# Kernel tuning notes

Hardware: AMD Instinct MI355X
Metric: run time of the kernel (lower is better)

Reference implementation:

```python
import math
import jax, jax.numpy as jnp
import numpy as np

B, L, D = 8, 512, 512          # batch, seq, d_model
G, S = 8, 4                    # n_groups, expert_scale (clones per group)
FG, FE = 4, 64                 # features per group, d_feat_emb
E = G * S                      # n_experts = 32
DH, RH = 256, 256              # d_expert_hidden, d_router_hidden
TEMP, SHARP, BIAS = 1.0, 16.0, 1.0
GK, SK = 2, 2                  # group_top_k, expert_top_k


def setup_inputs() -> dict:
    key = jax.random.key(0)
    ks = jax.random.split(key, 12)
    def n(k, shape, fan_in):
        return (jax.random.normal(k, shape) * (fan_in ** -0.5)).astype(jnp.float32)
    return {
        "hidden": jax.random.normal(ks[0], (B, L, D), jnp.float32),
        "feat": jax.random.uniform(ks[1], (B, L, G * FG), dtype=jnp.float32),
        "valid_mask": jnp.ones((B, L), jnp.bool_),
        # outer (group) router: hidden -> RH -> G
        "Wr1": n(ks[2], (D, RH), D), "br1": jnp.zeros((RH,), jnp.float32),
        "Wr2": n(ks[3], (RH, G), RH), "br2": jnp.zeros((G,), jnp.float32),
        # per-group feature embedding: FG -> FE
        "Wfe": n(ks[4], (G, FG, FE), FG), "bfe": jnp.zeros((G, FE), jnp.float32),
        # per-group inner (clone) router on [hidden ; feat_emb] -> S
        "Win_h": n(ks[5], (G, D, S), D + FE),
        "Win_f": n(ks[6], (G, FE, S), D + FE),
        "bin_b": jnp.zeros((G, S), jnp.float32),
        # per-expert MLP: D -> DH -> D
        "We1": n(ks[7], (E, D, DH), D), "be1": jnp.zeros((E, DH), jnp.float32),
        "We2": n(ks[8], (E, DH, D), DH), "be2": jnp.zeros((E, D), jnp.float32),
    }


def _to_ratio(x):
    # faithful to _to_ratio: clamp if already in [0,1], else Gaussian CDF
    clamped = jnp.clip(x, 0.0, 1.0)
    cdf = jnp.clip(0.5 * (1.0 + jax.lax.erf(x / math.sqrt(2.0))), 0.0, 1.0)
    in01 = jnp.logical_and(x.min() >= -1e-6, x.max() <= 1.0 + 1e-6)
    return jnp.where(in01, clamped, cdf)


def _topk_softmax(logits, k):
    # softmax over top-k entries, zeros elsewhere (== scatter of softmax(top_vals))
    vals, _ = jax.lax.top_k(logits, k)
    thresh = vals[..., -1:]
    neg = jnp.finfo(logits.dtype).min
    return jax.nn.softmax(jnp.where(logits >= thresh, logits, neg), axis=-1)


def _forward(hidden, feat, Wr1, br1, Wr2, br2, Wfe, bfe, Win_h, Win_f, bin_b,
             We1, be1, We2, be2):
    gelu = lambda x: jax.nn.gelu(x, approximate=False)  # torch nn.GELU default
    # ---- outer (group) router: hidden-only, token mode ----
    gh = gelu(hidden @ Wr1 + br1)                       # [B,L,RH]
    glog = (gh @ Wr2 + br2) / TEMP                      # [B,L,G]
    gw = _topk_softmax(glog, GK)                        # [B,L,G]
    # ---- inner rule teacher: bins over normalized group feature ratios ----
    feat_g = feat.reshape(B, L, G, FG)
    score = _to_ratio(feat_g).mean(-1, keepdims=True)   # [B,L,G,1]
    centers = jnp.linspace(0.0, 1.0, S, dtype=jnp.float32)
    rule = -SHARP * (score - centers) ** 2              # [B,L,G,S]
    # ---- inner (clone) router: hidden + group feature embedding + rule bias ----
    femb = jnp.einsum('blgf,gfe->blge', feat_g, Wfe) + bfe          # [B,L,G,FE]
    ilog = (jnp.einsum('bld,gds->blgs', hidden, Win_h)
            + jnp.einsum('blge,ges->blgs', femb, Win_f)
            + bin_b + BIAS * rule) / TEMP                            # [B,L,G,S]
    cw = _topk_softmax(ilog, SK)                                     # [B,L,G,S]
    # ---- combine hierarchical weights (group-major expert order) ----
    w = (gw[..., None] * cw).reshape(B, L, E)                        # [B,L,E]
    # ---- dense grouped expert MLPs (dropout=0 at eval) ----
    h1 = gelu(jnp.einsum('bld,edh->bleh', hidden, We1) + be1)        # [B,L,E,DH]
    y = jnp.einsum('bleh,ehd,ble->bld', h1, We2, w)
    y = y + jnp.einsum('ble,ed->bld', w, be2)
    return y


def reference(hidden, feat, valid_mask, Wr1, br1, Wr2, br2, Wfe, bfe,
              Win_h, Win_f, bin_b, We1, be1, We2, be2):
    del valid_mask  # token-mode routing; mask only used for session pooling
    return _forward(hidden, feat, Wr1, br1, Wr2, br2, Wfe, bfe,
                    Win_h, Win_f, bin_b, We1, be1, We2, be2)
```

## Files before the change

### kernel.cpp

```cpp
#include <hip/hip_runtime.h>
#include <hip/hip_bf16.h>
#include <math.h>

#define BB   8
#define LL   512
#define DD   512
#define GG   8
#define SSS  4
#define FGC  4
#define FEC  64
#define EEC  32
#define DHC  256
#define RHC  256
#define NT   (BB*LL)
#define TM   32
#define TR   8

#define XC_STRIDE 264
#define CPAD 32
#define NWL_MAX 4096
#define EGRID 1024
#define RBLK 512
#define PBLK 4096

typedef __attribute__((ext_vector_type(8))) short short8;
typedef __attribute__((ext_vector_type(4))) float floatx4;

__device__ __forceinline__ float gelu_exact(float x) {
    return 0.5f * x * (1.0f + erff(x * 0.70710678118654752440f));
}

__device__ __forceinline__ unsigned pk2(float a, float b) {
    union { __hip_bfloat162 h; unsigned u; } cv;
    cv.h = __float22bfloat162_rn(make_float2(a, b));
    return cv.u;
}
union U4S8 { unsigned u[4]; short8 s; };

__device__ __forceinline__ floatx4 mfma16(short8 a, short8 b, floatx4 c) {
    return __builtin_amdgcn_mfma_f32_16x16x32_bf16(a, b, c, 0, 0, 0);
}

__global__ __launch_bounds__(256) void prep_kernel(
    const float* __restrict__ Win_h, const float* __restrict__ Win_f,
    const float* __restrict__ Wfe, const float* __restrict__ bfe,
    const float* __restrict__ bin_b,
    float* __restrict__ WinT, float* __restrict__ M2, float* __restrict__ c2b)
{
    const int tid = threadIdx.x;
    if (blockIdx.x < 64) {
        int idx = blockIdx.x * 256 + tid;
        int d = idx >> 5, gs = idx & 31;
        int g = gs >> 2, s = gs & 3;
        WinT[idx] = Win_h[(size_t)g*DD*SSS + d*SSS + s];
    } else {
        if (tid < GG*FGC*SSS) {
            int g = tid >> 4, f = (tid >> 2) & 3, s = tid & 3;
            float acc = 0.f;
            for (int e = 0; e < FEC; ++e)
                acc += Wfe[(size_t)g*FGC*FEC + f*FEC + e] * Win_f[(size_t)g*FEC*SSS + e*SSS + s];
            M2[tid] = acc;
        } else if (tid < GG*FGC*SSS + GG*SSS) {
            int gs = tid - GG*FGC*SSS;
            int g = gs >> 2, s = gs & 3;
            float acc = bin_b[gs];
            for (int e = 0; e < FEC; ++e)
                acc += bfe[g*FEC + e] * Win_f[(size_t)g*FEC*SSS + e*SSS + s];
            c2b[gs] = acc;
        }
    }
}

__global__ __launch_bounds__(256) void route_and_pack(
    const float* __restrict__ hidden, const float* __restrict__ feat,
    const float* __restrict__ Wr1, const float* __restrict__ br1,
    const float* __restrict__ Wr2, const float* __restrict__ br2,
    const float* __restrict__ WinT, const float* __restrict__ M2,
    const float* __restrict__ c2b,
    int* __restrict__ bucket_tok, float* __restrict__ bucket_w,
    int* __restrict__ counts, int* __restrict__ nslot,
    const float* __restrict__ We1, const float* __restrict__ We2,
    short* __restrict__ Wp1, short* __restrict__ Wp2)
{
    const int tid = threadIdx.x;

    if (blockIdx.x >= RBLK) {
        const int gid = (blockIdx.x - RBLK) * 256 + tid;
        if (gid < EEC*16*16*64) {
            const int lane = gid & 63;
            const int nb   = (gid >> 6) & 15;
            const int i    = (gid >> 10) & 15;
            const int e    = gid >> 14;
            const int k0   = i*32 + (lane >> 4)*8;
            const int n    = nb*16 + (lane & 15);
            const float* s = We1 + ((size_t)e*DD + k0)*DHC + n;
            float f[8];
            #pragma unroll
            for (int j = 0; j < 8; ++j) f[j] = s[(size_t)j*DHC];
            U4S8 cv;
            cv.u[0] = pk2(f[0], f[1]); cv.u[1] = pk2(f[2], f[3]);
            cv.u[2] = pk2(f[4], f[5]); cv.u[3] = pk2(f[6], f[7]);
            *(short8*)(Wp1 + (size_t)gid*8) = cv.s;
        } else {
            const int g2   = gid - EEC*16*16*64;
            const int lane = g2 & 63;
            const int nb   = (g2 >> 6) & 31;
            const int i    = (g2 >> 11) & 7;
            const int e    = g2 >> 14;
            const int k0   = i*32 + (lane >> 4)*8;
            const int n    = nb*16 + (lane & 15);
            const float* s = We2 + ((size_t)e*DHC + k0)*DD + n;
            float f[8];
            #pragma unroll
            for (int j = 0; j < 8; ++j) f[j] = s[(size_t)j*DD];
            U4S8 cv;
            cv.u[0] = pk2(f[0], f[1]); cv.u[1] = pk2(f[2], f[3]);
            cv.u[2] = pk2(f[4], f[5]); cv.u[3] = pk2(f[6], f[7]);
            *(short8*)(Wp2 + (size_t)g2*8) = cv.s;
        }
        return;
    }

    const int t0 = blockIdx.x * TR;

    __shared__ float hs[TR][DD];
    __shared__ float ghs[TR][RHC+4];
    __shared__ float featb[TR][GG*FGC];
    __shared__ float glogp[TR][GG][4];
    __shared__ float gwvb[TR][GG];
    __shared__ float scoreb[TR][GG];
    __shared__ float ilogb[TR][GG*SSS];
    __shared__ float cwvb[TR][GG*SSS];

    for (int i = tid; i < TR*DD; i += 256) {
        int r = i >> 9, c = i & 511;
        hs[r][c] = hidden[(size_t)(t0 + r)*DD + c];
    }
    if (tid < TR*GG*FGC) {
        int r = tid >> 5, c = tid & 31;
        featb[r][c] = feat[(t0 + r)*(GG*FGC) + c];
    }
    __syncthreads();

    if (tid < TR*GG) {
        int t = tid >> 3, g = tid & 7;
        float s = 0.f;
        #pragma unroll
        for (int f = 0; f < FGC; ++f) s += fminf(fmaxf(featb[t][g*4+f], 0.f), 1.f);
        scoreb[t][g] = s * 0.25f;
    }

    {
        float acc[TR];
        float b = br1[tid];
        #pragma unroll
        for (int t = 0; t < TR; ++t) acc[t] = b;
        #pragma unroll 4
        for (int k = 0; k < DD; k += 4) {
            float w0 = Wr1[(size_t)k*RHC + tid];
            float w1 = Wr1[(size_t)(k+1)*RHC + tid];
            float w2 = Wr1[(size_t)(k+2)*RHC + tid];
            float w3 = Wr1[(size_t)(k+3)*RHC + tid];
            #pragma unroll
            for (int t = 0; t < TR; ++t) {
                float4 h = *(const float4*)(&hs[t][k]);
                acc[t] += h.x*w0 + h.y*w1 + h.z*w2 + h.w*w3;
            }
        }
        #pragma unroll
        for (int t = 0; t < TR; ++t) ghs[t][tid] = gelu_exact(acc[t]);
    }
    __syncthreads();

    {
        const int t = tid >> 5, g = (tid >> 2) & 7, q = tid & 3;
        float s = (q == 0) ? br2[g] : 0.f;
        const float* wr = Wr2 + g;
        #pragma unroll 4
        for (int h = q*64; h < q*64 + 64; ++h) s += ghs[t][h] * wr[(size_t)h*GG];
        glogp[t][g][q] = s;
    }

    {
        const int t = tid >> 5, gs = tid & 31;
        const int g = gs >> 2, s = gs & 3;
        float acc = 0.f;
        #pragma unroll 8
        for (int k = 0; k < DD; ++k) acc += hs[t][k] * WinT[k*32 + gs];
        const float* m2 = M2 + g*16 + s;
        acc += featb[t][g*4+0]*m2[0] + featb[t][g*4+1]*m2[4]
             + featb[t][g*4+2]*m2[8] + featb[t][g*4+3]*m2[12];
        const float centers[4] = {0.0f, 1.0f/3.0f, 2.0f/3.0f, 1.0f};
        float diff = scoreb[t][g] - centers[s];
        ilogb[t][gs] = acc + c2b[gs] - 16.0f * diff * diff;
    }
    __syncthreads();

    if (tid < TR) {
        int t = tid;
        float gl[GG];
        #pragma unroll
        for (int g = 0; g < GG; ++g)
            gl[g] = glogp[t][g][0] + glogp[t][g][1] + glogp[t][g][2] + glogp[t][g][3];
        float a = -INFINITY, b = -INFINITY;
        #pragma unroll
        for (int g = 0; g < GG; ++g) {
            float v = gl[g];
            if (v > a) { b = a; a = v; } else if (v > b) { b = v; }
        }
        float thresh = b, m = a, sum = 0.f;
        float ex[GG];
        #pragma unroll
        for (int g = 0; g < GG; ++g) {
            ex[g] = (gl[g] >= thresh) ? __expf(gl[g] - m) : 0.f;
            sum += ex[g];
        }
        float inv = 1.0f / sum;
        #pragma unroll
        for (int g = 0; g < GG; ++g) gwvb[t][g] = ex[g] * inv;
    }
    if (tid < TR*GG) {
        int t = tid >> 3, g = tid & 7;
        float vv[4] = {ilogb[t][g*4+0], ilogb[t][g*4+1], ilogb[t][g*4+2], ilogb[t][g*4+3]};
        float a = -INFINITY, b = -INFINITY;
        #pragma unroll
        for (int s = 0; s < 4; ++s) {
            float v = vv[s];
            if (v > a) { b = a; a = v; } else if (v > b) { b = v; }
        }
        float thresh = b, m = a, sum = 0.f;
        float ex[4];
        #pragma unroll
        for (int s = 0; s < 4; ++s) {
            ex[s] = (vv[s] >= thresh) ? __expf(vv[s] - m) : 0.f;
            sum += ex[s];
        }
        float inv = 1.0f / sum;
        #pragma unroll
        for (int s = 0; s < 4; ++s) cwvb[t][g*4 + s] = ex[s] * inv;
    }
    __syncthreads();

    if (tid < TR) {
        int t = tid;
        int a = 0;
        for (int g = 0; g < GG; ++g) {
            float gw = gwvb[t][g];
            if (gw > 0.f) {
                for (int s = 0; s < SSS; ++s) {
                    float w = gw * cwvb[t][g*4 + s];
                    if (w > 0.f && a < 4) {
                        int ee = g*SSS + s;
                        int pos = atomicAdd(&counts[ee*CPAD], 1);
                        bucket_tok[ee*NT + pos] = ((t0 + t) << 2) | a;
                        bucket_w[ee*NT + pos]   = w;
                        ++a;
                    }
                }
            }
        }
        nslot[t0 + t] = a;
    }
}

__global__ __launch_bounds__(64) void build_worklist(
    const int* __restrict__ counts, int* __restrict__ worklist,
    int* __restrict__ nwork)
{
    __shared__ int tiles[EEC], offs[EEC];
    const int tid = threadIdx.x;
    if (tid < EEC) tiles[tid] = (counts[tid*CPAD] + TM - 1) / TM;
    __syncthreads();
    if (tid == 0) {
        int acc = 0;
        for (int e = 0; e < EEC; ++e) { offs[e] = acc; acc += tiles[e]; }
        nwork[0] = acc;
    }
    __syncthreads();
    if (tid < EEC) {
        const int n = tiles[tid], o = offs[tid];
        for (int t = 0; t < n; ++t) worklist[o + t] = (tid << 16) | t;
    }
}

__global__ __launch_bounds__(256) void expert_mfma5(
    const float* __restrict__ hidden,
    const short* __restrict__ Wp1, const float* __restrict__ be1,
    const short* __restrict__ Wp2, const float* __restrict__ be2,
    const int* __restrict__ bucket_tok, const float* __restrict__ bucket_w,
    const int* __restrict__ counts,
    const int* __restrict__ worklist, const int* __restrict__ nwork,
    float* __restrict__ y_part)
{
    const int NW   = nwork[0];
    const int tid  = threadIdx.x;
    const int wave = tid >> 6;
    const int lane = tid & 63;
    const int lm   = lane & 15;
    const int quad = lane >> 4;

    __shared__ short Xp[64 * XC_STRIDE];
    __shared__ short Hp[32 * XC_STRIDE];
    __shared__ int   toks[TM];
    __shared__ float tws[TM];

    for (int it = blockIdx.x; it < NW; it += EGRID) {
        const int item = worklist[it];
        const int e    = item >> 16;
        const int tile = item & 0xffff;
        const int cnt  = counts[e*CPAD];
        const int r0   = tile * TM;
        const int nrow = min(TM, cnt - r0);

        const short* W1 = Wp1 + (size_t)e * (16*16*64*8);
        const short* W2 = Wp2 + (size_t)e * (8*32*64*8);

        if (tid < TM) {
            if (tid < nrow) {
                toks[tid] = bucket_tok[e*NT + r0 + tid];
                tws[tid]  = bucket_w[e*NT + r0 + tid];
            } else { toks[tid] = -1; tws[tid] = 0.f; }
        }

        short8 b1c[4];
        {
            const short* wb = W1 + ((size_t)wave*4)*512 + lane*8;
            #pragma unroll
            for (int nb = 0; nb < 4; ++nb) b1c[nb] = *(const short8*)(wb + nb*512);
        }
        __syncthreads();

        {
            const int xr = tid >> 3;
            const int xk = tid & 7;
            const int bt = toks[xr];
            const float* src = hidden + (size_t)(bt < 0 ? 0 : (bt >> 2))*DD;
            #pragma unroll
            for (int i = 0; i < 8; ++i) {
                const int k8 = xk + 8*i;
                float4 v0 = make_float4(0.f,0.f,0.f,0.f), v1 = v0;
                if (bt >= 0) {
                    v0 = *(const float4*)(src + k8*8);
                    v1 = *(const float4*)(src + k8*8 + 4);
                }
                U4S8 cv;
                cv.u[0] = pk2(v0.x, v0.y); cv.u[1] = pk2(v0.z, v0.w);
                cv.u[2] = pk2(v1.x, v1.y); cv.u[3] = pk2(v1.z, v1.w);
                *(short8*)(&Xp[k8 * XC_STRIDE + xr * 8]) = cv.s;
            }
        }
        __syncthreads();

        floatx4 acc[2][4];
        #pragma unroll
        for (int mb = 0; mb < 2; ++mb)
            #pragma unroll
            for (int nb = 0; nb < 4; ++nb)
                acc[mb][nb] = (floatx4){0.f, 0.f, 0.f, 0.f};

        for (int i = 0; i < 16; ++i) {
            const int k8 = i*4 + quad;
            short8 b1n[4];
            if (i < 15) {
                const short* wb = W1 + ((size_t)(i+1)*16 + wave*4)*512 + lane*8;
                #pragma unroll
                for (int nb = 0; nb < 4; ++nb) b1n[nb] = *(const short8*)(wb + nb*512);
            }
            short8 a0 = *(const short8*)(&Xp[k8 * XC_STRIDE + lm * 8]);
            short8 a1 = *(const short8*)(&Xp[k8 * XC_STRIDE + (16 + lm) * 8]);
            #pragma unroll
            for (int nb = 0; nb < 4; ++nb) {
                acc[0][nb] = mfma16(a0, b1c[nb], acc[0][nb]);
                acc[1][nb] = mfma16(a1, b1c[nb], acc[1][nb]);
            }
            if (i < 15) {
                #pragma unroll
                for (int nb = 0; nb < 4; ++nb) b1c[nb] = b1n[nb];
            }
        }

        short8 b2c[8];
        {
            const short* wb = W2 + ((size_t)wave*8)*512 + lane*8;
            #pragma unroll
            for (int nb = 0; nb < 8; ++nb) b2c[nb] = *(const short8*)(wb + nb*512);
        }

        #pragma unroll
        for (int nb = 0; nb < 4; ++nb) {
            const int h = wave*64 + nb*16 + lm;
            const float b1 = be1[e*DHC + h];
            #pragma unroll
            for (int mb = 0; mb < 2; ++mb) {
                #pragma unroll
                for (int r = 0; r < 4; r += 2) {
                    const int m0 = mb*16 + quad*4 + r;
                    unsigned u = pk2(gelu_exact(acc[mb][nb][r]   + b1),
                                     gelu_exact(acc[mb][nb][r+1] + b1));
                    Hp[(h >> 3) * XC_STRIDE + m0 * 8 + (h & 7)]     = (short)(u & 0xffff);
                    Hp[(h >> 3) * XC_STRIDE + (m0+1) * 8 + (h & 7)] = (short)(u >> 16);
                }
            }
        }
        __syncthreads();

        floatx4 c[2][8];
        #pragma unroll
        for (int mb = 0; mb < 2; ++mb)
            #pragma unroll
            for (int nb = 0; nb < 8; ++nb)
                c[mb][nb] = (floatx4){0.f, 0.f, 0.f, 0.f};

        for (int i = 0; i < 8; ++i) {
            const int k8 = i*4 + quad;
            short8 b2n[8];
            if (i < 7) {
                const short* wb = W2 + ((size_t)(i+1)*32 + wave*8)*512 + lane*8;
                #pragma unroll
                for (int nb = 0; nb < 8; ++nb) b2n[nb] = *(const short8*)(wb + nb*512);
            }
            short8 a0 = *(const short8*)(&Hp[k8 * XC_STRIDE + lm * 8]);
            short8 a1 = *(const short8*)(&Hp[k8 * XC_STRIDE + (16 + lm) * 8]);
            #pragma unroll
            for (int nb = 0; nb < 8; ++nb) {
                c[0][nb] = mfma16(a0, b2c[nb], c[0][nb]);
                c[1][nb] = mfma16(a1, b2c[nb], c[1][nb]);
            }
            if (i < 7) {
                #pragma unroll
                for (int nb = 0; nb < 8; ++nb) b2c[nb] = b2n[nb];
            }
        }

        #pragma unroll
        for (int nb = 0; nb < 8; ++nb) {
            const int col = wave*128 + nb*16 + lm;
            const float b2 = be2[e*DD + col];
            #pragma unroll
            for (int mb = 0; mb < 2; ++mb) {
                #pragma unroll
                for (int r = 0; r < 4; ++r) {
                    const int m = mb*16 + quad*4 + r;
                    const int bt = toks[m];
                    if (bt >= 0)
                        y_part[(size_t)bt*DD + col] = tws[m] * (c[mb][nb][r] + b2);
                }
            }
        }
        __syncthreads();
    }
}

__global__ __launch_bounds__(256) void reduce_y(
    const float* __restrict__ y_part, const int* __restrict__ nslot,
    float* __restrict__ y)
{
    const int idx = blockIdx.x * 256 + threadIdx.x;
    const int t  = idx >> 7;
    const int c4 = idx & 127;
    const int ns = nslot[t];
    float4 s = make_float4(0.f, 0.f, 0.f, 0.f);
    const float* p = y_part + ((size_t)t*4)*DD + c4*4;
    for (int a = 0; a < ns; ++a) {
        float4 v = *(const float4*)(p + (size_t)a*DD);
        s.x += v.x; s.y += v.y; s.z += v.z; s.w += v.w;
    }
    *(float4*)(y + (size_t)t*DD + c4*4) = s;
}

__global__ __launch_bounds__(256) void expert_mfma3(
    const float* __restrict__ hidden,
    const float* __restrict__ We1, const float* __restrict__ be1,
    const float* __restrict__ We2, const float* __restrict__ be2,
    const int* __restrict__ bucket_tok, const float* __restrict__ bucket_w,
    const int* __restrict__ counts,
    float* __restrict__ y)
{
    const int e    = blockIdx.x & 31;
    const int tile = blockIdx.x >> 5;
    const int cnt  = counts[e*CPAD];
    const int r0   = tile * TM;
    if (r0 >= cnt) return;
    const int nrow = min(TM, cnt - r0);
    const int tid  = threadIdx.x;
    const int wave = tid >> 6;
    const int lane = tid & 63;
    const int lm   = lane & 15;
    const int quad = lane >> 4;

    __shared__ short Xp[64 * XC_STRIDE];
    __shared__ short Hp[32 * XC_STRIDE];
    __shared__ int   toks[TM];
    __shared__ float tws[TM];

    if (tid < TM) {
        if (tid < nrow) {
            toks[tid] = bucket_tok[e*NT + r0 + tid] >> 2;
            tws[tid]  = bucket_w[e*NT + r0 + tid];
        } else { toks[tid] = -1; tws[tid] = 0.f; }
    }
    __syncthreads();

    {
        const int xr = tid >> 3;
        const int xk = tid & 7;
        const int tk = toks[xr];
        const float* src = hidden + (size_t)(tk < 0 ? 0 : tk)*DD;
        #pragma unroll
        for (int i = 0; i < 8; ++i) {
            const int k8 = xk + 8*i;
            float4 v0 = make_float4(0.f,0.f,0.f,0.f), v1 = v0;
            if (tk >= 0) {
                v0 = *(const float4*)(src + k8*8);
                v1 = *(const float4*)(src + k8*8 + 4);
            }
            U4S8 cv;
            cv.u[0] = pk2(v0.x, v0.y); cv.u[1] = pk2(v0.z, v0.w);
            cv.u[2] = pk2(v1.x, v1.y); cv.u[3] = pk2(v1.z, v1.w);
            *(short8*)(&Xp[k8 * XC_STRIDE + xr * 8]) = cv.s;
        }
    }
    __syncthreads();

    floatx4 acc[2][4];
    #pragma unroll
    for (int mb = 0; mb < 2; ++mb)
        #pragma unroll
        for (int nb = 0; nb < 4; ++nb)
            acc[mb][nb] = (floatx4){0.f, 0.f, 0.f, 0.f};

    const float* W1 = We1 + (size_t)e * DD * DHC;

    for (int i = 0; i < 16; ++i) {
        const int k8 = i*4 + quad;
        short8 a0 = *(const short8*)(&Xp[k8 * XC_STRIDE + lm * 8]);
        short8 a1 = *(const short8*)(&Xp[k8 * XC_STRIDE + (16 + lm) * 8]);
        float wreg[4][8];
        #pragma unroll
        for (int nb = 0; nb < 4; ++nb) {
            const float* s = W1 + (size_t)(k8*8)*DHC + wave*64 + nb*16 + lm;
            #pragma unroll
            for (int j = 0; j < 8; ++j) wreg[nb][j] = s[(size_t)j*DHC];
        }
        #pragma unroll
        for (int nb = 0; nb < 4; ++nb) {
            U4S8 cv;
            cv.u[0] = pk2(wreg[nb][0], wreg[nb][1]);
            cv.u[1] = pk2(wreg[nb][2], wreg[nb][3]);
            cv.u[2] = pk2(wreg[nb][4], wreg[nb][5]);
            cv.u[3] = pk2(wreg[nb][6], wreg[nb][7]);
            acc[0][nb] = mfma16(a0, cv.s, acc[0][nb]);
            acc[1][nb] = mfma16(a1, cv.s, acc[1][nb]);
        }
    }

    #pragma unroll
    for (int nb = 0; nb < 4; ++nb) {
        const int h = wave*64 + nb*16 + lm;
        const float b1 = be1[e*DHC + h];
        #pragma unroll
        for (int mb = 0; mb < 2; ++mb) {
            #pragma unroll
            for (int r = 0; r < 4; r += 2) {
                const int m0 = mb*16 + quad*4 + r;
                unsigned u = pk2(gelu_exact(acc[mb][nb][r]   + b1),
                                 gelu_exact(acc[mb][nb][r+1] + b1));
                Hp[(h >> 3) * XC_STRIDE + m0 * 8 + (h & 7)]     = (short)(u & 0xffff);
                Hp[(h >> 3) * XC_STRIDE + (m0+1) * 8 + (h & 7)] = (short)(u >> 16);
            }
        }
    }
    __syncthreads();

    floatx4 c[2][8];
    #pragma unroll
    for (int mb = 0; mb < 2; ++mb)
        #pragma unroll
        for (int nb = 0; nb < 8; ++nb)
            c[mb][nb] = (floatx4){0.f, 0.f, 0.f, 0.f};

    const float* W2 = We2 + (size_t)e * DHC * DD;

    for (int i = 0; i < 8; ++i) {
        const int k8 = i*4 + quad;
        short8 a0 = *(const short8*)(&Hp[k8 * XC_STRIDE + lm * 8]);
        short8 a1 = *(const short8*)(&Hp[k8 * XC_STRIDE + (16 + lm) * 8]);
        #pragma unroll
        for (int half = 0; half < 2; ++half) {
            float wreg[4][8];
            #pragma unroll
            for (int nb4 = 0; nb4 < 4; ++nb4) {
                const int n = wave*128 + (half*4 + nb4)*16 + lm;
                const float* s = W2 + (size_t)(k8*8)*DD + n;
                #pragma unroll
                for (int j = 0; j < 8; ++j) wreg[nb4][j] = s[(size_t)j*DD];
            }
            #pragma unroll
            for (int nb4 = 0; nb4 < 4; ++nb4) {
                const int nb = half*4 + nb4;
                U4S8 cv;
                cv.u[0] = pk2(wreg[nb4][0], wreg[nb4][1]);
                cv.u[1] = pk2(wreg[nb4][2], wreg[nb4][3]);
                cv.u[2] = pk2(wreg[nb4][4], wreg[nb4][5]);
                cv.u[3] = pk2(wreg[nb4][6], wreg[nb4][7]);
                c[0][nb] = mfma16(a0, cv.s, c[0][nb]);
                c[1][nb] = mfma16(a1, cv.s, c[1][nb]);
            }
        }
    }

    #pragma unroll
    for (int nb = 0; nb < 8; ++nb) {
        const int col = wave*128 + nb*16 + lm;
        const float b2 = be2[e*DD + col];
        #pragma unroll
        for (int mb = 0; mb < 2; ++mb) {
            #pragma unroll
            for (int r = 0; r < 4; ++r) {
                const int m = mb*16 + quad*4 + r;
                const int tk = toks[m];
                if (tk >= 0)
                    atomicAdd(&y[(size_t)tk*DD + col], tws[m] * (c[mb][nb][r] + b2));
            }
        }
    }
}

extern "C" void kernel_launch(void* const* d_in, const int* in_sizes, int n_in,
                              void* d_out, int out_size, void* d_ws, size_t ws_size,
                              hipStream_t stream) {
    const float* hidden = (const float*)d_in[0];
    const float* feat   = (const float*)d_in[1];
    const float* Wr1    = (const float*)d_in[3];
    const float* br1    = (const float*)d_in[4];
    const float* Wr2    = (const float*)d_in[5];
    const float* br2    = (const float*)d_in[6];
    const float* Wfe    = (const float*)d_in[7];
    const float* bfe    = (const float*)d_in[8];
    const float* Win_h  = (const float*)d_in[9];
    const float* Win_f  = (const float*)d_in[10];
    const float* bin_b  = (const float*)d_in[11];
    const float* We1    = (const float*)d_in[12];
    const float* be1    = (const float*)d_in[13];
    const float* We2    = (const float*)d_in[14];
    const float* be2    = (const float*)d_in[15];
    float* y = (float*)d_out;

    char* ws = (char*)d_ws;
    int*   bucket_tok = (int*)ws;    ws += (size_t)EEC*NT*sizeof(int);
    float* bucket_w   = (float*)ws;  ws += (size_t)EEC*NT*sizeof(float);
    int*   counts     = (int*)ws;    ws += (size_t)EEC*CPAD*sizeof(int);
    float* WinT       = (float*)ws;  ws += (size_t)DD*EEC*sizeof(float);
    float* M2         = (float*)ws;  ws += 512;
    float* c2b        = (float*)ws;  ws += 256;
    int*   nslot      = (int*)ws;    ws += (size_t)NT*sizeof(int);
    int*   worklist   = (int*)ws;    ws += (size_t)NWL_MAX*sizeof(int);
    int*   nwork      = (int*)ws;    ws += 128;
    size_t base_used  = (size_t)(ws - (char*)d_ws);

    short* Wp1    = (short*)ws;
    short* Wp2    = Wp1 + (size_t)EEC*DD*DHC;
    float* y_part = (float*)(Wp2 + (size_t)EEC*DHC*DD);
    size_t need_fast = base_used
                     + 2*(size_t)EEC*DD*DHC*sizeof(short)
                     + (size_t)NT*4*DD*sizeof(float);
    const bool fast = (ws_size >= need_fast);

    hipMemsetAsync(counts, 0, EEC*CPAD*sizeof(int), stream);

    prep_kernel<<<65, 256, 0, stream>>>(Win_h, Win_f, Wfe, bfe, bin_b,
                                        WinT, M2, c2b);

    if (fast) {
        route_and_pack<<<RBLK + PBLK, 256, 0, stream>>>(
            hidden, feat, Wr1, br1, Wr2, br2, WinT, M2, c2b,
            bucket_tok, bucket_w, counts, nslot,
            We1, We2, Wp1, Wp2);

        build_worklist<<<1, 64, 0, stream>>>(counts, worklist, nwork);

        expert_mfma5<<<EGRID, 256, 0, stream>>>(hidden, Wp1, be1, Wp2, be2,
                                                bucket_tok, bucket_w, counts,
                                                worklist, nwork, y_part);

        reduce_y<<<(NT*DD/4)/256, 256, 0, stream>>>(y_part, nslot, y);
    } else {
        hipMemsetAsync(y, 0, (size_t)NT*DD*sizeof(float), stream);

        route_and_pack<<<RBLK, 256, 0, stream>>>(
            hidden, feat, Wr1, br1, Wr2, br2, WinT, M2, c2b,
            bucket_tok, bucket_w, counts, nslot,
            We1, We2, (short*)nullptr, (short*)nullptr);

        expert_mfma3<<<(NT/TM)*EEC, 256, 0, stream>>>(hidden, We1, be1, We2, be2,
                                                      bucket_tok, bucket_w, counts, y);
    }
}
```

Measured before the change: 258.1 us.

## Split router K-loop across 512 threads and fold worklist build into last block

```diff
diff --git a/kernel.cpp b/kernel.cpp
--- a/kernel.cpp
+++ b/kernel.cpp
@@ -21,7 +21,7 @@
 #define NWL_MAX 4096
 #define EGRID 1024
 #define RBLK 512
-#define PBLK 4096
+#define PBLK 2048
 
 typedef __attribute__((ext_vector_type(8))) short short8;
 typedef __attribute__((ext_vector_type(4))) float floatx4;
@@ -71,7 +71,7 @@
     }
 }
 
-__global__ __launch_bounds__(256) void route_and_pack(
+__global__ __launch_bounds__(512) void route_and_pack(
     const float* __restrict__ hidden, const float* __restrict__ feat,
     const float* __restrict__ Wr1, const float* __restrict__ br1,
     const float* __restrict__ Wr2, const float* __restrict__ br2,
@@ -80,12 +80,14 @@
     int* __restrict__ bucket_tok, float* __restrict__ bucket_w,
     int* __restrict__ counts, int* __restrict__ nslot,
     const float* __restrict__ We1, const float* __restrict__ We2,
-    short* __restrict__ Wp1, short* __restrict__ Wp2)
+    short* __restrict__ Wp1, short* __restrict__ Wp2,
+    int* __restrict__ rdone, int* __restrict__ worklist,
+    int* __restrict__ nwork)
 {
     const int tid = threadIdx.x;
 
     if (blockIdx.x >= RBLK) {
-        const int gid = (blockIdx.x - RBLK) * 256 + tid;
+        const int gid = (blockIdx.x - RBLK) * 512 + tid;
         if (gid < EEC*16*16*64) {
             const int lane = gid & 63;
             const int nb   = (gid >> 6) & 15;
@@ -125,14 +127,16 @@
 
     __shared__ float hs[TR][DD];
     __shared__ float ghs[TR][RHC+4];
+    __shared__ float pgh[2][TR][RHC];
     __shared__ float featb[TR][GG*FGC];
     __shared__ float glogp[TR][GG][4];
     __shared__ float gwvb[TR][GG];
     __shared__ float scoreb[TR][GG];
     __shared__ float ilogb[TR][GG*SSS];
     __shared__ float cwvb[TR][GG*SSS];
-
-    for (int i = tid; i < TR*DD; i += 256) {
+    __shared__ int   isLast;
+
+    for (int i = tid; i < TR*DD; i += 512) {
         int r = i >> 9, c = i & 511;
         hs[r][c] = hidden[(size_t)(t0 + r)*DD + c];
     }
@@ -151,38 +155,47 @@
     }
 
     {
+        const int h  = tid & 255;
+        const int kh = tid >> 8;
         float acc[TR];
-        float b = br1[tid];
+        float b = (kh == 0) ? br1[h] : 0.f;
         #pragma unroll
         for (int t = 0; t < TR; ++t) acc[t] = b;
+        const int k0 = kh * 256;
         #pragma unroll 4
-        for (int k = 0; k < DD; k += 4) {
-            float w0 = Wr1[(size_t)k*RHC + tid];
-            float w1 = Wr1[(size_t)(k+1)*RHC + tid];
-            float w2 = Wr1[(size_t)(k+2)*RHC + tid];
-            float w3 = Wr1[(size_t)(k+3)*RHC + tid];
+        for (int k = k0; k < k0 + 256; k += 4) {
+            float w0 = Wr1[(size_t)k*RHC + h];
+            float w1 = Wr1[(size_t)(k+1)*RHC + h];
+            float w2 = Wr1[(size_t)(k+2)*RHC + h];
+            float w3 = Wr1[(size_t)(k+3)*RHC + h];
             #pragma unroll
             for (int t = 0; t < TR; ++t) {
-                float4 h = *(const float4*)(&hs[t][k]);
-                acc[t] += h.x*w0 + h.y*w1 + h.z*w2 + h.w*w3;
-            }
-        }
-        #pragma unroll
-        for (int t = 0; t < TR; ++t) ghs[t][tid] = gelu_exact(acc[t]);
-    }
-    __syncthreads();
-
-    {
+                float4 hv = *(const float4*)(&hs[t][k]);
+                acc[t] += hv.x*w0 + hv.y*w1 + hv.z*w2 + hv.w*w3;
+            }
+        }
+        #pragma unroll
+        for (int t = 0; t < TR; ++t) pgh[kh][t][h] = acc[t];
+    }
+    __syncthreads();
+
+    if (tid < RHC) {
+        #pragma unroll
+        for (int t = 0; t < TR; ++t)
+            ghs[t][tid] = gelu_exact(pgh[0][t][tid] + pgh[1][t][tid]);
+    }
+    __syncthreads();
+
+    if (tid < 256) {
         const int t = tid >> 5, g = (tid >> 2) & 7, q = tid & 3;
         float s = (q == 0) ? br2[g] : 0.f;
         const float* wr = Wr2 + g;
         #pragma unroll 4
         for (int h = q*64; h < q*64 + 64; ++h) s += ghs[t][h] * wr[(size_t)h*GG];
         glogp[t][g][q] = s;
-    }
-
-    {
-        const int t = tid >> 5, gs = tid & 31;
+    } else {
+        const int tid2 = tid - 256;
+        const int t = tid2 >> 5, gs = tid2 & 31;
         const int g = gs >> 2, s = gs & 3;
         float acc = 0.f;
         #pragma unroll 8
@@ -261,25 +274,28 @@
         }
         nslot[t0 + t] = a;
     }
-}
-
-__global__ __launch_bounds__(64) void build_worklist(
-    const int* __restrict__ counts, int* __restrict__ worklist,
-    int* __restrict__ nwork)
-{
-    __shared__ int tiles[EEC], offs[EEC];
-    const int tid = threadIdx.x;
-    if (tid < EEC) tiles[tid] = (counts[tid*CPAD] + TM - 1) / TM;
+
     __syncthreads();
     if (tid == 0) {
-        int acc = 0;
-        for (int e = 0; e < EEC; ++e) { offs[e] = acc; acc += tiles[e]; }
-        nwork[0] = acc;
-    }
-    __syncthreads();
-    if (tid < EEC) {
-        const int n = tiles[tid], o = offs[tid];
-        for (int t = 0; t < n; ++t) worklist[o + t] = (tid << 16) | t;
+        __threadfence();
+        isLast = (atomicAdd(rdone, 1) == RBLK - 1) ? 1 : 0;
+    }
+    __syncthreads();
+    if (isLast) {
+        __shared__ int tiles[EEC], offs[EEC];
+        if (tid < EEC)
+            tiles[tid] = (atomicAdd(&counts[tid*CPAD], 0) + TM - 1) / TM;
+        __syncthreads();
+        if (tid == 0) {
+            int acc = 0;
+            for (int e = 0; e < EEC; ++e) { offs[e] = acc; acc += tiles[e]; }
+            nwork[0] = acc;
+        }
+        __syncthreads();
+        if (tid < EEC) {
+            const int n = tiles[tid], o = offs[tid];
+            for (int t = 0; t < n; ++t) worklist[o + t] = (tid << 16) | t;
+        }
     }
 }
 
@@ -650,6 +666,7 @@
     int*   bucket_tok = (int*)ws;    ws += (size_t)EEC*NT*sizeof(int);
     float* bucket_w   = (float*)ws;  ws += (size_t)EEC*NT*sizeof(float);
     int*   counts     = (int*)ws;    ws += (size_t)EEC*CPAD*sizeof(int);
+    int*   rdone      = (int*)ws;    ws += 128;
     float* WinT       = (float*)ws;  ws += (size_t)DD*EEC*sizeof(float);
     float* M2         = (float*)ws;  ws += 512;
     float* c2b        = (float*)ws;  ws += 256;
@@ -666,18 +683,16 @@
                      + (size_t)NT*4*DD*sizeof(float);
     const bool fast = (ws_size >= need_fast);
 
-    hipMemsetAsync(counts, 0, EEC*CPAD*sizeof(int), stream);
+    hipMemsetAsync(counts, 0, EEC*CPAD*sizeof(int) + 128, stream);
 
     prep_kernel<<<65, 256, 0, stream>>>(Win_h, Win_f, Wfe, bfe, bin_b,
                                         WinT, M2, c2b);
 
     if (fast) {
-        route_and_pack<<<RBLK + PBLK, 256, 0, stream>>>(
+        route_and_pack<<<RBLK + PBLK, 512, 0, stream>>>(
             hidden, feat, Wr1, br1, Wr2, br2, WinT, M2, c2b,
             bucket_tok, bucket_w, counts, nslot,
-            We1, We2, Wp1, Wp2);
-
-        build_worklist<<<1, 64, 0, stream>>>(counts, worklist, nwork);
+            We1, We2, Wp1, Wp2, rdone, worklist, nwork);
 
         expert_mfma5<<<EGRID, 256, 0, stream>>>(hidden, Wp1, be1, Wp2, be2,
                                                 bucket_tok, bucket_w, counts,
@@ -687,10 +702,10 @@
     } else {
         hipMemsetAsync(y, 0, (size_t)NT*DD*sizeof(float), stream);
 
-        route_and_pack<<<RBLK, 256, 0, stream>>>(
+        route_and_pack<<<RBLK, 512, 0, stream>>>(
             hidden, feat, Wr1, br1, Wr2, br2, WinT, M2, c2b,
             bucket_tok, bucket_w, counts, nslot,
-            We1, We2, (short*)nullptr, (short*)nullptr);
+            We1, We2, (short*)nullptr, (short*)nullptr, rdone, worklist, nwork);
 
         expert_mfma3<<<(NT/TM)*EEC, 256, 0, stream>>>(hidden, We1, be1, We2, be2,
                                                       bucket_tok, bucket_w, counts, y);
```

Result: slower. 285.7 us (+10.7%).

## Fuse worklist build into routing kernel via last-block atomic, retile router GEMV

Applied to the files above, without the earlier changes.

```diff
diff --git a/kernel.cpp b/kernel.cpp
--- a/kernel.cpp
+++ b/kernel.cpp
@@ -80,7 +80,9 @@
     int* __restrict__ bucket_tok, float* __restrict__ bucket_w,
     int* __restrict__ counts, int* __restrict__ nslot,
     const float* __restrict__ We1, const float* __restrict__ We2,
-    short* __restrict__ Wp1, short* __restrict__ Wp2)
+    short* __restrict__ Wp1, short* __restrict__ Wp2,
+    int* __restrict__ rdone, int* __restrict__ worklist,
+    int* __restrict__ nwork)
 {
     const int tid = threadIdx.x;
 
@@ -131,6 +133,7 @@
     __shared__ float scoreb[TR][GG];
     __shared__ float ilogb[TR][GG*SSS];
     __shared__ float cwvb[TR][GG*SSS];
+    __shared__ int   isLast;
 
     for (int i = tid; i < TR*DD; i += 256) {
         int r = i >> 9, c = i & 511;
@@ -151,24 +154,30 @@
     }
 
     {
-        float acc[TR];
-        float b = br1[tid];
-        #pragma unroll
-        for (int t = 0; t < TR; ++t) acc[t] = b;
+        const int th = tid >> 7;
+        const int c0 = (tid & 127) * 2;
+        float acc0[4], acc1[4];
+        const float bb0 = br1[c0], bb1 = br1[c0 + 1];
+        #pragma unroll
+        for (int t = 0; t < 4; ++t) { acc0[t] = bb0; acc1[t] = bb1; }
         #pragma unroll 4
         for (int k = 0; k < DD; k += 4) {
-            float w0 = Wr1[(size_t)k*RHC + tid];
-            float w1 = Wr1[(size_t)(k+1)*RHC + tid];
-            float w2 = Wr1[(size_t)(k+2)*RHC + tid];
-            float w3 = Wr1[(size_t)(k+3)*RHC + tid];
-            #pragma unroll
-            for (int t = 0; t < TR; ++t) {
-                float4 h = *(const float4*)(&hs[t][k]);
-                acc[t] += h.x*w0 + h.y*w1 + h.z*w2 + h.w*w3;
-            }
-        }
-        #pragma unroll
-        for (int t = 0; t < TR; ++t) ghs[t][tid] = gelu_exact(acc[t]);
+            float2 w0 = *(const float2*)(&Wr1[(size_t)k*RHC + c0]);
+            float2 w1 = *(const float2*)(&Wr1[(size_t)(k+1)*RHC + c0]);
+            float2 w2 = *(const float2*)(&Wr1[(size_t)(k+2)*RHC + c0]);
+            float2 w3 = *(const float2*)(&Wr1[(size_t)(k+3)*RHC + c0]);
+            #pragma unroll
+            for (int t = 0; t < 4; ++t) {
+                float4 h = *(const float4*)(&hs[th*4 + t][k]);
+                acc0[t] += h.x*w0.x + h.y*w1.x + h.z*w2.x + h.w*w3.x;
+                acc1[t] += h.x*w0.y + h.y*w1.y + h.z*w2.y + h.w*w3.y;
+            }
+        }
+        #pragma unroll
+        for (int t = 0; t < 4; ++t) {
+            ghs[th*4 + t][c0]     = gelu_exact(acc0[t]);
+            ghs[th*4 + t][c0 + 1] = gelu_exact(acc1[t]);
+        }
     }
     __syncthreads();
 
@@ -261,25 +270,28 @@
         }
         nslot[t0 + t] = a;
     }
-}
-
-__global__ __launch_bounds__(64) void build_worklist(
-    const int* __restrict__ counts, int* __restrict__ worklist,
-    int* __restrict__ nwork)
-{
-    __shared__ int tiles[EEC], offs[EEC];
-    const int tid = threadIdx.x;
-    if (tid < EEC) tiles[tid] = (counts[tid*CPAD] + TM - 1) / TM;
+
     __syncthreads();
     if (tid == 0) {
-        int acc = 0;
-        for (int e = 0; e < EEC; ++e) { offs[e] = acc; acc += tiles[e]; }
-        nwork[0] = acc;
-    }
-    __syncthreads();
-    if (tid < EEC) {
-        const int n = tiles[tid], o = offs[tid];
-        for (int t = 0; t < n; ++t) worklist[o + t] = (tid << 16) | t;
+        __threadfence();
+        isLast = (atomicAdd(rdone, 1) == RBLK - 1) ? 1 : 0;
+    }
+    __syncthreads();
+    if (isLast) {
+        __shared__ int tiles[EEC], offs[EEC];
+        if (tid < EEC)
+            tiles[tid] = (atomicAdd(&counts[tid*CPAD], 0) + TM - 1) / TM;
+        __syncthreads();
+        if (tid == 0) {
+            int acc = 0;
+            for (int e = 0; e < EEC; ++e) { offs[e] = acc; acc += tiles[e]; }
+            nwork[0] = acc;
+        }
+        __syncthreads();
+        if (tid < EEC) {
+            const int n = tiles[tid], o = offs[tid];
+            for (int t = 0; t < n; ++t) worklist[o + t] = (tid << 16) | t;
+        }
     }
 }
 
@@ -650,6 +662,7 @@
     int*   bucket_tok = (int*)ws;    ws += (size_t)EEC*NT*sizeof(int);
     float* bucket_w   = (float*)ws;  ws += (size_t)EEC*NT*sizeof(float);
     int*   counts     = (int*)ws;    ws += (size_t)EEC*CPAD*sizeof(int);
+    int*   rdone      = (int*)ws;    ws += 128;
     float* WinT       = (float*)ws;  ws += (size_t)DD*EEC*sizeof(float);
     float* M2         = (float*)ws;  ws += 512;
     float* c2b        = (float*)ws;  ws += 256;
@@ -666,7 +679,7 @@
                      + (size_t)NT*4*DD*sizeof(float);
     const bool fast = (ws_size >= need_fast);
 
-    hipMemsetAsync(counts, 0, EEC*CPAD*sizeof(int), stream);
+    hipMemsetAsync(counts, 0, EEC*CPAD*sizeof(int) + 128, stream);
 
     prep_kernel<<<65, 256, 0, stream>>>(Win_h, Win_f, Wfe, bfe, bin_b,
                                         WinT, M2, c2b);
@@ -675,9 +688,7 @@
         route_and_pack<<<RBLK + PBLK, 256, 0, stream>>>(
             hidden, feat, Wr1, br1, Wr2, br2, WinT, M2, c2b,
             bucket_tok, bucket_w, counts, nslot,
-            We1, We2, Wp1, Wp2);
-
-        build_worklist<<<1, 64, 0, stream>>>(counts, worklist, nwork);
+            We1, We2, Wp1, Wp2, rdone, worklist, nwork);
 
         expert_mfma5<<<EGRID, 256, 0, stream>>>(hidden, Wp1, be1, Wp2, be2,
                                                 bucket_tok, bucket_w, counts,
@@ -690,7 +701,7 @@
         route_and_pack<<<RBLK, 256, 0, stream>>>(
             hidden, feat, Wr1, br1, Wr2, br2, WinT, M2, c2b,
             bucket_tok, bucket_w, counts, nslot,
-            We1, We2, (short*)nullptr, (short*)nullptr);
+            We1, We2, (short*)nullptr, (short*)nullptr, rdone, worklist, nwork);
 
         expert_mfma3<<<(NT/TM)*EEC, 256, 0, stream>>>(hidden, We1, be1, We2, be2,
                                                       bucket_tok, bucket_w, counts, y);
```

After: 260.2 us. Within noise of the previous version (+0.8%).
